# Performance work log

Measured on AMD Instinct MI355X. Metric: run time of the kernel, lower is better.

## Reference

```python
import jax, jax.numpy as jnp
from jax import lax
import numpy as np

B, D, L = 262144, 64, 10


def setup_inputs() -> dict:
    key = jax.random.key(0)
    k1, k2, k3, k4, k5 = jax.random.split(key, 5)
    inputs = jax.random.normal(k1, (B, 1), dtype=jnp.float32)  # only batch dim is used
    Q = jax.random.uniform(k2, (D * (D - 1) // 2,), minval=-0.01, maxval=0.01, dtype=jnp.float32)
    delta = jax.random.uniform(k3, (D,), minval=-1.0, maxval=1.0, dtype=jnp.float32)
    # initial spins: sign of uniform(-1, 1), as in the keras layer
    x0 = jnp.sign(jax.random.uniform(k4, (B, D), minval=-1.0, maxval=1.0, dtype=jnp.float32))
    # per-sweep, per-coordinate uniform noise u ~ U[0,1)
    u = jax.random.uniform(k5, (L, B, D), dtype=jnp.float32)
    return {"inputs": inputs, "Q": Q, "delta": delta, "x0": x0, "u": u,
            "n_layers": L, "const": 10}


def _build_M(Q, dim):
    # scatter Q into strict lower triangle (row-major, k1>k2), then symmetrize
    rows, cols = np.tril_indices(dim, -1)
    M = jnp.zeros((dim, dim), Q.dtype).at[rows, cols].set(Q)
    return M + M.T


def reference(inputs, Q, delta, x0, u, n_layers, const):
    dim = delta.shape[0]
    M = _build_M(Q, dim)
    c = jnp.asarray(const, x0.dtype)

    def sweep(x, u_l):  # one Gauss-Seidel Gibbs sweep; x: (B, D), u_l: (B, D)
        def body(x, k):
            # M[k,k] == 0, so Gauss-Seidel reduces to a matvec against current x
            alpha = delta[k] + x @ M[k]                      # (B,)
            # exp(a)/(exp(a)+exp(-a)) == sigmoid(2a)
            new = jnp.tanh(c * (jax.nn.sigmoid(2.0 * alpha) - u_l[:, k]))
            return x.at[:, k].set(new), None
        x, _ = lax.scan(body, x, jnp.arange(dim))
        return x, None

    z, _ = lax.scan(sweep, x0, u)                            # (B, D)
    energy = jnp.sum(0.5 * (z @ M) * z + delta * z, -1)      # (B,)
    return z, energy
```

## Files before the change

### kernel.cpp

```cpp
#include <hip/hip_runtime.h>

#define DD 64
#define HALF 32
#define STRIDE 33

__global__ void build_M_kernel(const float* __restrict__ Q, float* __restrict__ M) {
    int idx = blockIdx.x * 256 + threadIdx.x;
    if (idx < DD * DD) {
        int r = idx >> 6;
        int c = idx & 63;
        float v = 0.0f;
        if (r > c)      v = Q[(r * (r - 1)) / 2 + c];
        else if (c > r) v = Q[(c * (c - 1)) / 2 + r];
        M[idx] = v;
    }
}

__device__ __forceinline__ float fast_sigmoid2(float alpha) {
    float e = __expf(-2.0f * fabsf(alpha));
    float r = __builtin_amdgcn_rcpf(1.0f + e);
    return (alpha >= 0.0f) ? r : e * r;
}

__device__ __forceinline__ float fast_tanh(float t) {
    float a = fabsf(t);
    float e = __expf(-2.0f * a);
    float r = (1.0f - e) * __builtin_amdgcn_rcpf(1.0f + e);
    return copysignf(r, t);
}

template<int K>
__device__ __forceinline__ void gs_step(float (&x)[DD],
        const float* __restrict__ M, const float* __restrict__ delta,
        float c, const float* __restrict__ s_u)
{
    const float* Mr = M + K * DD;
    float a0 = 0.f, a1 = 0.f, a2 = 0.f, a3 = 0.f;
#pragma unroll
    for (int j = 0; j < DD; j += 4) {
        a0 = fmaf(Mr[j + 0], x[j + 0], a0);
        a1 = fmaf(Mr[j + 1], x[j + 1], a1);
        a2 = fmaf(Mr[j + 2], x[j + 2], a2);
        a3 = fmaf(Mr[j + 3], x[j + 3], a3);
    }
    float alpha = delta[K] + ((a0 + a1) + (a2 + a3));
    float uk = s_u[K & (HALF - 1)];
    x[K] = fast_tanh(c * (fast_sigmoid2(alpha) - uk));
}

template<int K, int KEND>
struct SweepChunk {
    static __device__ __forceinline__ void run(float (&x)[DD],
        const float* __restrict__ M, const float* __restrict__ delta,
        float c, const float* __restrict__ s_u)
    {
        gs_step<K>(x, M, delta, c, s_u);
        SweepChunk<K + 1, KEND>::run(x, M, delta, c, s_u);
    }
};
template<int KEND>
struct SweepChunk<KEND, KEND> {
    static __device__ __forceinline__ void run(float (&)[DD],
        const float*, const float*, float, const float*) {}
};

template<int K>
__device__ __forceinline__ float energy_step(const float (&x)[DD],
        const float* __restrict__ M, const float* __restrict__ delta)
{
    const float* Mr = M + K * DD;
    float a0 = 0.f, a1 = 0.f, a2 = 0.f, a3 = 0.f;
#pragma unroll
    for (int j = 0; j < DD; j += 4) {
        a0 = fmaf(Mr[j + 0], x[j + 0], a0);
        a1 = fmaf(Mr[j + 1], x[j + 1], a1);
        a2 = fmaf(Mr[j + 2], x[j + 2], a2);
        a3 = fmaf(Mr[j + 3], x[j + 3], a3);
    }
    float dot = (a0 + a1) + (a2 + a3);
    return (0.5f * dot + delta[K]) * x[K];
}

template<int K, int KEND>
struct EnergyAcc {
    static __device__ __forceinline__ float run(const float (&x)[DD],
        const float* __restrict__ M, const float* __restrict__ delta)
    {
        return energy_step<K>(x, M, delta) + EnergyAcc<K + 1, KEND>::run(x, M, delta);
    }
};
template<int KEND>
struct EnergyAcc<KEND, KEND> {
    static __device__ __forceinline__ float run(const float (&)[DD],
        const float*, const float*) { return 0.0f; }
};

template<int CH, int J>
struct LoadX {
    static __device__ __forceinline__ void run(float (&x)[DD], const float* __restrict__ s_row) {
        x[CH * HALF + J] = s_row[J];
        LoadX<CH, J + 1>::run(x, s_row);
    }
};
template<int CH>
struct LoadX<CH, HALF> {
    static __device__ __forceinline__ void run(float (&)[DD], const float*) {}
};

template<int CH, int J>
struct StoreX {
    static __device__ __forceinline__ void run(const float (&x)[DD], float* __restrict__ s_row) {
        s_row[J] = x[CH * HALF + J];
        StoreX<CH, J + 1>::run(x, s_row);
    }
};
template<int CH>
struct StoreX<CH, HALF> {
    static __device__ __forceinline__ void run(const float (&)[DD], float*) {}
};

__device__ __forceinline__ void stage_chunk(const float* __restrict__ gsrc,
                                            float* __restrict__ s_buf, int t)
{
#pragma unroll
    for (int it = 0; it < 8; ++it) {
        int g = it * 256 + t;
        int r = g >> 3;
        int q = g & 7;
        float4 v = *(const float4*)(gsrc + (size_t)r * DD + q * 4);
        float* d = s_buf + r * STRIDE + q * 4;
        d[0] = v.x; d[1] = v.y; d[2] = v.z; d[3] = v.w;
    }
}

__device__ __forceinline__ void unstage_chunk(float* __restrict__ gdst,
                                              const float* __restrict__ s_buf, int t)
{
#pragma unroll
    for (int it = 0; it < 8; ++it) {
        int g = it * 256 + t;
        int r = g >> 3;
        int q = g & 7;
        const float* s = s_buf + r * STRIDE + q * 4;
        *(float4*)(gdst + (size_t)r * DD + q * 4) = make_float4(s[0], s[1], s[2], s[3]);
    }
}

__global__ __launch_bounds__(256, 3) void ising_main(
    const float* __restrict__ M,
    const float* __restrict__ delta,
    const float* __restrict__ x0,
    const float* __restrict__ u,
    const int* __restrict__ n_layers_p,
    const int* __restrict__ const_p,
    float* __restrict__ out,
    int B)
{
    __shared__ float s_buf[256 * STRIDE];

    const int t  = threadIdx.x;
    const int b0 = blockIdx.x * 256;
    const int b  = b0 + t;
    const int L = n_layers_p[0];
    const float c = (float)const_p[0];

    float x[DD];
    float* s_row = s_buf + t * STRIDE;

    stage_chunk(x0 + (size_t)b0 * DD + 0, s_buf, t);
    __syncthreads();
    LoadX<0, 0>::run(x, s_row);
    __syncthreads();
    stage_chunk(x0 + (size_t)b0 * DD + HALF, s_buf, t);
    __syncthreads();
    LoadX<1, 0>::run(x, s_row);
    __syncthreads();

    for (int l = 0; l < L; ++l) {
        const float* ub = u + ((size_t)l * B + b0) * DD;
        stage_chunk(ub, s_buf, t);
        __syncthreads();
        SweepChunk<0, HALF>::run(x, M, delta, c, s_row);
        __syncthreads();
        stage_chunk(ub + HALF, s_buf, t);
        __syncthreads();
        SweepChunk<HALF, DD>::run(x, M, delta, c, s_row);
        __syncthreads();
    }

    float energy = EnergyAcc<0, DD>::run(x, M, delta);

    StoreX<0, 0>::run(x, s_row);
    __syncthreads();
    unstage_chunk(out + (size_t)b0 * DD + 0, s_buf, t);
    __syncthreads();
    StoreX<1, 0>::run(x, s_row);
    __syncthreads();
    unstage_chunk(out + (size_t)b0 * DD + HALF, s_buf, t);

    out[(size_t)B * DD + b] = energy;
}

extern "C" void kernel_launch(void* const* d_in, const int* in_sizes, int n_in,
                              void* d_out, int out_size, void* d_ws, size_t ws_size,
                              hipStream_t stream) {
    const float* Q     = (const float*)d_in[1];
    const float* delta = (const float*)d_in[2];
    const float* x0    = (const float*)d_in[3];
    const float* u     = (const float*)d_in[4];
    const int*   nl    = (const int*)d_in[5];
    const int*   cc    = (const int*)d_in[6];
    float* M = (float*)d_ws;
    int B = in_sizes[3] / DD;

    build_M_kernel<<<(DD * DD + 255) / 256, 256, 0, stream>>>(Q, M);
    ising_main<<<B / 256, 256, 0, stream>>>(M, delta, x0, u, nl, cc,
                                            (float*)d_out, B);
}
```

Baseline: 1.954 ms.

## Use packed FMA dot products, direct per-thread loads, and simplified activation math

Stores the spin state as float2 vectors so each matvec step can issue packed FMAs (v_pk_fma_f32) with M rows read as float2. The LDS staging and barriers for x0, u and the output are removed: each thread now reads its own u rows and writes its own output rows with float4 accesses. The sigmoid/tanh chain is rewritten with exp2 and a pre-scaled u (tanh(y) = 1 - 2/(1+exp(2y))), and launch bounds rise to 4 blocks per CU. The risks are uncoalesced per-thread 256-byte strided global accesses and higher register pressure under the tighter occupancy bound.

After: 1.643 ms. -15.9%, faster.

```diff
diff --git a/kernel.cpp b/kernel.cpp
--- a/kernel.cpp
+++ b/kernel.cpp
@@ -1,8 +1,9 @@
 #include <hip/hip_runtime.h>
 
 #define DD 64
-#define HALF 32
-#define STRIDE 33
+
+typedef float v2f __attribute__((ext_vector_type(2)));
+typedef float v4f __attribute__((ext_vector_type(4)));
 
 __global__ void build_M_kernel(const float* __restrict__ Q, float* __restrict__ M) {
     int idx = blockIdx.x * 256 + threadIdx.x;
@@ -16,137 +17,87 @@
     }
 }
 
-__device__ __forceinline__ float fast_sigmoid2(float alpha) {
-    float e = __expf(-2.0f * fabsf(alpha));
-    float r = __builtin_amdgcn_rcpf(1.0f + e);
-    return (alpha >= 0.0f) ? r : e * r;
+template<int K>
+__device__ __forceinline__ void gs_step(v2f (&x)[32],
+        const float* __restrict__ M, const float* __restrict__ delta,
+        float k2, const v4f (&uc)[8])
+{
+    const v2f* __restrict__ Mr = (const v2f*)(M + K * DD);
+    v2f a0 = {0.f, 0.f}, a1 = {0.f, 0.f}, a2 = {0.f, 0.f}, a3 = {0.f, 0.f};
+#pragma unroll
+    for (int j = 0; j < 32; j += 4) {
+        a0 = __builtin_elementwise_fma(Mr[j + 0], x[j + 0], a0);
+        a1 = __builtin_elementwise_fma(Mr[j + 1], x[j + 1], a1);
+        a2 = __builtin_elementwise_fma(Mr[j + 2], x[j + 2], a2);
+        a3 = __builtin_elementwise_fma(Mr[j + 3], x[j + 3], a3);
+    }
+    v2f s = (a0 + a1) + (a2 + a3);
+    float alpha = (s[0] + s[1]) + delta[K];
+    const float NEG2LOG2E = -2.8853900817779268f;
+    float sig = __builtin_amdgcn_rcpf(1.0f + exp2f(alpha * NEG2LOG2E));
+    float r = __builtin_amdgcn_rcpf(1.0f + exp2f(fmaf(sig, k2, -uc[(K & 31) >> 2][K & 3])));
+    x[K >> 1][K & 1] = fmaf(-2.0f, r, 1.0f);
 }
 
-__device__ __forceinline__ float fast_tanh(float t) {
-    float a = fabsf(t);
-    float e = __expf(-2.0f * a);
-    float r = (1.0f - e) * __builtin_amdgcn_rcpf(1.0f + e);
-    return copysignf(r, t);
+template<int K, int KEND>
+struct Steps {
+    static __device__ __forceinline__ void run(v2f (&x)[32],
+            const float* __restrict__ M, const float* __restrict__ delta,
+            float k2, const v4f (&uc)[8]) {
+        gs_step<K>(x, M, delta, k2, uc);
+        Steps<K + 1, KEND>::run(x, M, delta, k2, uc);
+    }
+};
+template<int KEND>
+struct Steps<KEND, KEND> {
+    static __device__ __forceinline__ void run(v2f (&)[32],
+            const float*, const float*, float, const v4f (&)[8]) {}
+};
+
+template<int H>
+__device__ __forceinline__ void half_sweep(v2f (&x)[32],
+        const float* __restrict__ M, const float* __restrict__ delta,
+        float k2, const float* __restrict__ ub)
+{
+    const v4f* __restrict__ up = (const v4f*)(ub + H * 32);
+    v4f uc[8];
+#pragma unroll
+    for (int i = 0; i < 8; ++i) uc[i] = up[i] * k2;
+    Steps<H * 32, H * 32 + 32>::run(x, M, delta, k2, uc);
 }
 
 template<int K>
-__device__ __forceinline__ void gs_step(float (&x)[DD],
-        const float* __restrict__ M, const float* __restrict__ delta,
-        float c, const float* __restrict__ s_u)
-{
-    const float* Mr = M + K * DD;
-    float a0 = 0.f, a1 = 0.f, a2 = 0.f, a3 = 0.f;
-#pragma unroll
-    for (int j = 0; j < DD; j += 4) {
-        a0 = fmaf(Mr[j + 0], x[j + 0], a0);
-        a1 = fmaf(Mr[j + 1], x[j + 1], a1);
-        a2 = fmaf(Mr[j + 2], x[j + 2], a2);
-        a3 = fmaf(Mr[j + 3], x[j + 3], a3);
-    }
-    float alpha = delta[K] + ((a0 + a1) + (a2 + a3));
-    float uk = s_u[K & (HALF - 1)];
-    x[K] = fast_tanh(c * (fast_sigmoid2(alpha) - uk));
-}
-
-template<int K, int KEND>
-struct SweepChunk {
-    static __device__ __forceinline__ void run(float (&x)[DD],
-        const float* __restrict__ M, const float* __restrict__ delta,
-        float c, const float* __restrict__ s_u)
-    {
-        gs_step<K>(x, M, delta, c, s_u);
-        SweepChunk<K + 1, KEND>::run(x, M, delta, c, s_u);
-    }
-};
-template<int KEND>
-struct SweepChunk<KEND, KEND> {
-    static __device__ __forceinline__ void run(float (&)[DD],
-        const float*, const float*, float, const float*) {}
-};
-
-template<int K>
-__device__ __forceinline__ float energy_step(const float (&x)[DD],
+__device__ __forceinline__ float energy_step(const v2f (&x)[32],
         const float* __restrict__ M, const float* __restrict__ delta)
 {
-    const float* Mr = M + K * DD;
-    float a0 = 0.f, a1 = 0.f, a2 = 0.f, a3 = 0.f;
+    const v2f* __restrict__ Mr = (const v2f*)(M + K * DD);
+    v2f a0 = {0.f, 0.f}, a1 = {0.f, 0.f}, a2 = {0.f, 0.f}, a3 = {0.f, 0.f};
 #pragma unroll
-    for (int j = 0; j < DD; j += 4) {
-        a0 = fmaf(Mr[j + 0], x[j + 0], a0);
-        a1 = fmaf(Mr[j + 1], x[j + 1], a1);
-        a2 = fmaf(Mr[j + 2], x[j + 2], a2);
-        a3 = fmaf(Mr[j + 3], x[j + 3], a3);
+    for (int j = 0; j < 32; j += 4) {
+        a0 = __builtin_elementwise_fma(Mr[j + 0], x[j + 0], a0);
+        a1 = __builtin_elementwise_fma(Mr[j + 1], x[j + 1], a1);
+        a2 = __builtin_elementwise_fma(Mr[j + 2], x[j + 2], a2);
+        a3 = __builtin_elementwise_fma(Mr[j + 3], x[j + 3], a3);
     }
-    float dot = (a0 + a1) + (a2 + a3);
-    return (0.5f * dot + delta[K]) * x[K];
+    v2f s = (a0 + a1) + (a2 + a3);
+    float dot = s[0] + s[1];
+    return fmaf(0.5f, dot, delta[K]) * x[K >> 1][K & 1];
 }
 
 template<int K, int KEND>
 struct EnergyAcc {
-    static __device__ __forceinline__ float run(const float (&x)[DD],
-        const float* __restrict__ M, const float* __restrict__ delta)
-    {
+    static __device__ __forceinline__ float run(const v2f (&x)[32],
+            const float* __restrict__ M, const float* __restrict__ delta) {
         return energy_step<K>(x, M, delta) + EnergyAcc<K + 1, KEND>::run(x, M, delta);
     }
 };
 template<int KEND>
 struct EnergyAcc<KEND, KEND> {
-    static __device__ __forceinline__ float run(const float (&)[DD],
-        const float*, const float*) { return 0.0f; }
+    static __device__ __forceinline__ float run(const v2f (&)[32],
+            const float*, const float*) { return 0.0f; }
 };
 
-template<int CH, int J>
-struct LoadX {
-    static __device__ __forceinline__ void run(float (&x)[DD], const float* __restrict__ s_row) {
-        x[CH * HALF + J] = s_row[J];
-        LoadX<CH, J + 1>::run(x, s_row);
-    }
-};
-template<int CH>
-struct LoadX<CH, HALF> {
-    static __device__ __forceinline__ void run(float (&)[DD], const float*) {}
-};
-
-template<int CH, int J>
-struct StoreX {
-    static __device__ __forceinline__ void run(const float (&x)[DD], float* __restrict__ s_row) {
-        s_row[J] = x[CH * HALF + J];
-        StoreX<CH, J + 1>::run(x, s_row);
-    }
-};
-template<int CH>
-struct StoreX<CH, HALF> {
-    static __device__ __forceinline__ void run(const float (&)[DD], float*) {}
-};
-
-__device__ __forceinline__ void stage_chunk(const float* __restrict__ gsrc,
-                                            float* __restrict__ s_buf, int t)
-{
-#pragma unroll
-    for (int it = 0; it < 8; ++it) {
-        int g = it * 256 + t;
-        int r = g >> 3;
-        int q = g & 7;
-        float4 v = *(const float4*)(gsrc + (size_t)r * DD + q * 4);
-        float* d = s_buf + r * STRIDE + q * 4;
-        d[0] = v.x; d[1] = v.y; d[2] = v.z; d[3] = v.w;
-    }
-}
-
-__device__ __forceinline__ void unstage_chunk(float* __restrict__ gdst,
-                                              const float* __restrict__ s_buf, int t)
-{
-#pragma unroll
-    for (int it = 0; it < 8; ++it) {
-        int g = it * 256 + t;
-        int r = g >> 3;
-        int q = g & 7;
-        const float* s = s_buf + r * STRIDE + q * 4;
-        *(float4*)(gdst + (size_t)r * DD + q * 4) = make_float4(s[0], s[1], s[2], s[3]);
-    }
-}
-
-__global__ __launch_bounds__(256, 3) void ising_main(
+__global__ __launch_bounds__(256, 4) void ising_main(
     const float* __restrict__ M,
     const float* __restrict__ delta,
     const float* __restrict__ x0,
@@ -156,48 +107,37 @@
     float* __restrict__ out,
     int B)
 {
-    __shared__ float s_buf[256 * STRIDE];
-
-    const int t  = threadIdx.x;
-    const int b0 = blockIdx.x * 256;
-    const int b  = b0 + t;
+    const int b = blockIdx.x * 256 + threadIdx.x;
     const int L = n_layers_p[0];
     const float c = (float)const_p[0];
+    const float k2 = 2.0f * c * 1.4426950408889634f;
 
-    float x[DD];
-    float* s_row = s_buf + t * STRIDE;
-
-    stage_chunk(x0 + (size_t)b0 * DD + 0, s_buf, t);
-    __syncthreads();
-    LoadX<0, 0>::run(x, s_row);
-    __syncthreads();
-    stage_chunk(x0 + (size_t)b0 * DD + HALF, s_buf, t);
-    __syncthreads();
-    LoadX<1, 0>::run(x, s_row);
-    __syncthreads();
+    v2f x[32];
+    {
+        const v4f* __restrict__ xs = (const v4f*)(x0 + (size_t)b * DD);
+#pragma unroll
+        for (int i = 0; i < 16; ++i) {
+            v4f v = xs[i];
+            x[2 * i]     = (v2f){v[0], v[1]};
+            x[2 * i + 1] = (v2f){v[2], v[3]};
+        }
+    }
 
     for (int l = 0; l < L; ++l) {
-        const float* ub = u + ((size_t)l * B + b0) * DD;
-        stage_chunk(ub, s_buf, t);
-        __syncthreads();
-        SweepChunk<0, HALF>::run(x, M, delta, c, s_row);
-        __syncthreads();
-        stage_chunk(ub + HALF, s_buf, t);
-        __syncthreads();
-        SweepChunk<HALF, DD>::run(x, M, delta, c, s_row);
-        __syncthreads();
+        const float* __restrict__ ub = u + ((size_t)l * B + b) * (size_t)DD;
+        half_sweep<0>(x, M, delta, k2, ub);
+        half_sweep<1>(x, M, delta, k2, ub);
     }
 
     float energy = EnergyAcc<0, DD>::run(x, M, delta);
 
-    StoreX<0, 0>::run(x, s_row);
-    __syncthreads();
-    unstage_chunk(out + (size_t)b0 * DD + 0, s_buf, t);
-    __syncthreads();
-    StoreX<1, 0>::run(x, s_row);
-    __syncthreads();
-    unstage_chunk(out + (size_t)b0 * DD + HALF, s_buf, t);
-
+    {
+        v4f* __restrict__ zd = (v4f*)(out + (size_t)b * DD);
+#pragma unroll
+        for (int i = 0; i < 16; ++i) {
+            zd[i] = (v4f){x[2 * i][0], x[2 * i][1], x[2 * i + 1][0], x[2 * i + 1][1]};
+        }
+    }
     out[(size_t)B * DD + b] = energy;
 }
 
```
